# Performance work log

Measured on AMD Instinct MI355X. Metric: run time of the kernel, lower is better.

## Reference

```python
import jax, jax.numpy as jnp
import numpy as np

E = 2048        # embedding_dim
H = 16          # num_q_heads
G = 4           # group_size
HKV = H // G    # num_kv_heads = 4
D = E // H      # q_head_dim = 128
KVD = E // G    # kv_head_dim = 512
B, N = 2, 2048


def setup_inputs() -> dict:
    key = jax.random.key(0)
    ks = jax.random.split(key, 5)
    s = 0.02
    return {
        "x": jax.random.normal(ks[0], (B, N, E), jnp.float32),
        "Wq": jax.random.normal(ks[1], (E, E), jnp.float32) * s,
        "Wk": jax.random.normal(ks[2], (KVD, E), jnp.float32) * s,
        "Wv": jax.random.normal(ks[3], (KVD, E), jnp.float32) * s,
        "Wo": jax.random.normal(ks[4], (E, E), jnp.float32) * s,
    }


def reference(x, Wq, Wk, Wv, Wo):
    b, n, _ = x.shape
    # projections (nn.Linear: y = x @ W.T)
    q = x @ Wq.T                              # (b, n, E)
    k = x @ Wk.T                              # (b, n, KVD)
    v = x @ Wv.T                              # (b, n, KVD)
    # split heads: q -> b h n d with h=H, then (h g) -> g,h layout
    q = q.reshape(b, n, H, D).transpose(0, 2, 1, 3)          # b H n d
    q = q.reshape(b, HKV, G, n, D).transpose(0, 2, 1, 3, 4)  # b g h n d  (h=HKV)
    k = k.reshape(b, n, HKV, D).transpose(0, 2, 1, 3)        # b h s d
    v = v.reshape(b, n, HKV, D).transpose(0, 2, 1, 3)        # b h s d
    scale = 1.0 / jnp.sqrt(jnp.asarray(D, x.dtype))
    scores = jnp.einsum('bghnd,bhsd->bghns', q, k) * scale   # full score tensor
    scores = jax.nn.softmax(scores, axis=-1)
    # dropout p=0.0 -> identity
    o = jnp.einsum('bghns,bhsd->bghnd', scores, v)           # b g h n d
    # rearrange 'b g h n d -> b n (h g) d' then concat heads
    o = o.transpose(0, 3, 2, 1, 4).reshape(b, n, E)          # b n (h g) d -> b n E
    return o @ Wo.T
```

## Files before the change

### kernel.cpp

```cpp
#include <hip/hip_runtime.h>
#include <hip/hip_bf16.h>
#include <cstdint>
#include <cstddef>

using u16 = unsigned short;
typedef __bf16 bf16x8 __attribute__((ext_vector_type(8)));
typedef float f32x4 __attribute__((ext_vector_type(4)));
typedef float f32x16 __attribute__((ext_vector_type(16)));
typedef u16 u16x4 __attribute__((ext_vector_type(4)));
typedef u16 u16x8 __attribute__((ext_vector_type(8)));
typedef uint32_t u32x4 __attribute__((ext_vector_type(4)));

__device__ __forceinline__ u16 f2bf(float f) {
  uint32_t u = __builtin_bit_cast(uint32_t, f);
  u += 0x7FFFu + ((u >> 16) & 1u);
  return (u16)(u >> 16);
}

__device__ __forceinline__ void gld_lds16(const void* g, void* l) {
  __builtin_amdgcn_global_load_lds(
      (const __attribute__((address_space(1))) unsigned int*)g,
      (__attribute__((address_space(3))) unsigned int*)l, 16, 0, 0);
}

#define MFMA16(a, b, c) __builtin_amdgcn_mfma_f32_16x16x32_bf16((a), (b), (c), 0, 0, 0)
#define MFMA32(a, b, c) __builtin_amdgcn_mfma_f32_32x32x16_bf16((a), (b), (c), 0, 0, 0)

__device__ __forceinline__ uint32_t pkbf(float a, float b) {
  uint32_t d;
  asm("v_cvt_pk_bf16_f32 %0, %1, %2" : "=v"(d) : "v"(a), "v"(b));
  return d;
}
__device__ __forceinline__ void swap32(uint32_t& a, uint32_t& b) {
  asm volatile("v_permlane32_swap_b32 %0, %1" : "+v"(a), "+v"(b));
}

__global__ void cvt_kernel(const float* __restrict__ in, u16* __restrict__ out, int n4) {
  int i = blockIdx.x * blockDim.x + threadIdx.x;
  int stride = gridDim.x * blockDim.x;
  for (; i < n4; i += stride) {
    float4 v = reinterpret_cast<const float4*>(in)[i];
    u16x4 o;
    o[0] = f2bf(v.x); o[1] = f2bf(v.y); o[2] = f2bf(v.z); o[3] = f2bf(v.w);
    reinterpret_cast<u16x4*>(out)[i] = o;
  }
}

template <bool OUT_BF16>
__global__ __launch_bounds__(256) void gemm_bt(const u16* __restrict__ A,
                                               const u16* __restrict__ B,
                                               void* __restrict__ Cv,
                                               int M, int N, int K) {
  __shared__ __align__(16) u16 Ash[128 * 32];
  __shared__ __align__(16) u16 Bsh[128 * 32];
  const int tid = threadIdx.x;
  const int w = tid >> 6, lane = tid & 63, ql = lane & 15, g = lane >> 4;
  const int wr = w >> 1, wc = w & 1;
  const int m0 = blockIdx.y * 128, n0 = blockIdx.x * 128;
  const int srow = w * 16 + (lane >> 2);
  const int sk = (lane & 3) * 8;
  const u16* Abase = A + (size_t)(m0 + srow) * K + sk;
  const u16* Bbase = B + (size_t)(n0 + srow) * K + sk;

  f32x4 acc[4][4];
#pragma unroll
  for (int i = 0; i < 4; i++)
#pragma unroll
    for (int j = 0; j < 4; j++) acc[i][j] = f32x4{0.f, 0.f, 0.f, 0.f};

  for (int kt = 0; kt < K; kt += 32) {
    gld_lds16(Abase + kt,                  Ash + w * 512);
    gld_lds16(Abase + (size_t)64 * K + kt, Ash + 2048 + w * 512);
    gld_lds16(Bbase + kt,                  Bsh + w * 512);
    gld_lds16(Bbase + (size_t)64 * K + kt, Bsh + 2048 + w * 512);
    __syncthreads();
    bf16x8 af[4], bfr[4];
#pragma unroll
    for (int i = 0; i < 4; i++)
      af[i] = *reinterpret_cast<const bf16x8*>(&Ash[(wr * 64 + i * 16 + ql) * 32 + g * 8]);
#pragma unroll
    for (int j = 0; j < 4; j++)
      bfr[j] = *reinterpret_cast<const bf16x8*>(&Bsh[(wc * 64 + j * 16 + ql) * 32 + g * 8]);
#pragma unroll
    for (int i = 0; i < 4; i++)
#pragma unroll
      for (int j = 0; j < 4; j++)
        acc[i][j] = MFMA16(af[i], bfr[j], acc[i][j]);
    __syncthreads();
  }

#pragma unroll
  for (int i = 0; i < 4; i++)
#pragma unroll
    for (int j = 0; j < 4; j++)
#pragma unroll
      for (int r = 0; r < 4; r++) {
        const int row = m0 + wr * 64 + i * 16 + g * 4 + r;
        const int col = n0 + wc * 64 + j * 16 + ql;
        if constexpr (OUT_BF16)
          ((u16*)Cv)[(size_t)row * N + col] = f2bf(acc[i][j][r]);
        else
          ((float*)Cv)[(size_t)row * N + col] = acc[i][j][r];
      }
}

__global__ __launch_bounds__(256, 2) void attn_kernel(const u16* __restrict__ QKV,
                                                      u16* __restrict__ O) {
  __shared__ __align__(16) u16 Kb[2][64 * 128];
  __shared__ __align__(16) u16 Vb[2][2][128 * 32];
  const int tid = threadIdx.x, w = tid >> 6, lane = tid & 63;
  const int lq = lane & 31, hi = lane >> 5;
  const int qt = blockIdx.x;
  const int b = blockIdx.y >> 4, h = blockIdx.y & 15, hkv = h >> 2;
  const size_t rowb = (size_t)b * 2048;
  const int qbase = qt * 128 + w * 32;

  const u16* Kg = QKV + 2048 + hkv * 128;
  const u16* Vg = QKV + 2560 + hkv * 128;

  bf16x8 bq[8];
  {
    const u16* qp = QKV + (rowb + qbase + lq) * 3072 + h * 128 + hi * 8;
#pragma unroll
    for (int s5 = 0; s5 < 8; s5++)
      bq[s5] = *reinterpret_cast<const bf16x8*>(qp + s5 * 16);
  }

  const int dg = tid & 7, sl = tid >> 3;

  f32x16 oacc[4];
#pragma unroll
  for (int dt = 0; dt < 4; dt++)
#pragma unroll
    for (int i = 0; i < 16; i++) oacc[dt][i] = 0.f;
  float m = -INFINITY, l = 0.f;
  const float CEXP = 0.08838834764831845f * 1.4426950408889634f;

  auto stageK = [&](int pb2, int sbase) {
#pragma unroll
    for (int p = 0; p < 4; p++) {
      const int L = p * 2048 + tid * 8;
      const int s = L >> 7;
      const int gI = (L >> 3) & 15;
      gld_lds16(Kg + (rowb + sbase + s) * 3072 + ((gI ^ (s & 7)) << 3),
                &Kb[pb2][p * 2048 + w * 512]);
    }
  };
  auto writeV = [&](int pb2, const u16x8& a00, const u16x8& a01,
                    const u16x8& a10, const u16x8& a11) {
#pragma unroll
    for (int sh2 = 0; sh2 < 2; sh2++)
#pragma unroll
      for (int hf = 0; hf < 2; hf++) {
        const u16x8 v = sh2 ? (hf ? a11 : a10) : (hf ? a01 : a00);
#pragma unroll
        for (int j = 0; j < 8; j++) {
          const int d = dg * 16 + hf * 8 + j;
          const int key = ((d >> 1) ^ (d >> 4)) & 3;
          Vb[pb2][sh2][d * 32 + (sl ^ (key << 3))] = v[j];
        }
      }
  };

#define KFRAG(PB, SH, S5) \
  (*reinterpret_cast<const bf16x8*>(&Kb[PB][((SH)*32 + lq) * 128 + ((((S5)*2 + hi) ^ (lq & 7)) << 3)]))
#define VFRAG(PB, DT, SS) \
  (*reinterpret_cast<const bf16x8*>(&Vb[PB][(SS) >> 1][((DT)*32 + lq) * 32 + \
      ((((SS) & 1) * 16 + hi * 8) ^ (((((DT)*32 + lq) >> 1) ^ (((DT)*32 + lq) >> 4)) & 3) << 3)]))

  u16x8 v00, v01, v10, v11;
  {
    const u16* vp = Vg + (rowb + sl) * 3072 + dg * 16;
    v00 = *reinterpret_cast<const u16x8*>(vp);
    v01 = *reinterpret_cast<const u16x8*>(vp + 8);
    const u16* vp2 = vp + (size_t)32 * 3072;
    v10 = *reinterpret_cast<const u16x8*>(vp2);
    v11 = *reinterpret_cast<const u16x8*>(vp2 + 8);
  }
  stageK(0, 0);
  writeV(0, v00, v01, v10, v11);
  __syncthreads();

#pragma unroll 1
  for (int sb = 0; sb < 32; sb++) {
    const int pb = sb & 1;
    if (sb < 31) {
      const u16* vp = Vg + (rowb + (sb + 1) * 64 + sl) * 3072 + dg * 16;
      v00 = *reinterpret_cast<const u16x8*>(vp);
      v01 = *reinterpret_cast<const u16x8*>(vp + 8);
      const u16* vp2 = vp + (size_t)32 * 3072;
      v10 = *reinterpret_cast<const u16x8*>(vp2);
      v11 = *reinterpret_cast<const u16x8*>(vp2 + 8);
      stageK(pb ^ 1, (sb + 1) * 64);
    }

    f32x16 sc0, sc1;
#pragma unroll
    for (int i = 0; i < 16; i++) { sc0[i] = 0.f; sc1[i] = 0.f; }
    __builtin_amdgcn_s_setprio(1);
#pragma unroll
    for (int s5 = 0; s5 < 8; s5++) {
      sc0 = MFMA32(KFRAG(pb, 0, s5), bq[s5], sc0);
      sc1 = MFMA32(KFRAG(pb, 1, s5), bq[s5], sc1);
    }
    __builtin_amdgcn_s_setprio(0);

    float u[16];
#pragma unroll
    for (int i = 0; i < 16; i++) u[i] = fmaxf(sc0[i], sc1[i]);
#pragma unroll
    for (int i = 0; i < 8; i++) u[i] = fmaxf(u[i], u[i + 8]);
#pragma unroll
    for (int i = 0; i < 4; i++) u[i] = fmaxf(u[i], u[i + 4]);
    float mx = fmaxf(fmaxf(u[0], u[1]), fmaxf(u[2], u[3]));
    mx = fmaxf(mx, __shfl_xor(mx, 32));

    if (__any((mx - m) * CEXP > 8.0f)) {
      const float mn = fmaxf(m, mx);
      const float corr = exp2f((m - mn) * CEXP);
      l *= corr;
#pragma unroll
      for (int dt = 0; dt < 4; dt++)
#pragma unroll
        for (int i = 0; i < 16; i++) oacc[dt][i] *= corr;
      m = mn;
    }

    const float mC = m * CEXP;
    float e0[16], e1[16];
#pragma unroll
    for (int i = 0; i < 16; i++) {
      e0[i] = exp2f(fmaf(sc0[i], CEXP, -mC));
      e1[i] = exp2f(fmaf(sc1[i], CEXP, -mC));
    }
    float s[16];
#pragma unroll
    for (int i = 0; i < 16; i++) s[i] = e0[i] + e1[i];
#pragma unroll
    for (int i = 0; i < 8; i++) s[i] = s[i] + s[i + 8];
#pragma unroll
    for (int i = 0; i < 4; i++) s[i] = s[i] + s[i + 4];
    float ps = (s[0] + s[1]) + (s[2] + s[3]);
    ps += __shfl_xor(ps, 32);
    l += ps;

    bf16x8 pf0, pf1, pf2, pf3;
    {
      uint32_t a, bw;
      u32x4 f;
      a = pkbf(e0[0], e0[1]);  bw = pkbf(e0[4], e0[5]);  swap32(a, bw);
      f[0] = a; f[2] = bw;
      a = pkbf(e0[2], e0[3]);  bw = pkbf(e0[6], e0[7]);  swap32(a, bw);
      f[1] = a; f[3] = bw;
      pf0 = __builtin_bit_cast(bf16x8, f);
      a = pkbf(e0[8], e0[9]);  bw = pkbf(e0[12], e0[13]); swap32(a, bw);
      f[0] = a; f[2] = bw;
      a = pkbf(e0[10], e0[11]); bw = pkbf(e0[14], e0[15]); swap32(a, bw);
      f[1] = a; f[3] = bw;
      pf1 = __builtin_bit_cast(bf16x8, f);
      a = pkbf(e1[0], e1[1]);  bw = pkbf(e1[4], e1[5]);  swap32(a, bw);
      f[0] = a; f[2] = bw;
      a = pkbf(e1[2], e1[3]);  bw = pkbf(e1[6], e1[7]);  swap32(a, bw);
      f[1] = a; f[3] = bw;
      pf2 = __builtin_bit_cast(bf16x8, f);
      a = pkbf(e1[8], e1[9]);  bw = pkbf(e1[12], e1[13]); swap32(a, bw);
      f[0] = a; f[2] = bw;
      a = pkbf(e1[10], e1[11]); bw = pkbf(e1[14], e1[15]); swap32(a, bw);
      f[1] = a; f[3] = bw;
      pf3 = __builtin_bit_cast(bf16x8, f);
    }

    __builtin_amdgcn_s_setprio(1);
#pragma unroll
    for (int dt = 0; dt < 4; dt++) {
      oacc[dt] = MFMA32(VFRAG(pb, dt, 0), pf0, oacc[dt]);
      oacc[dt] = MFMA32(VFRAG(pb, dt, 1), pf1, oacc[dt]);
      oacc[dt] = MFMA32(VFRAG(pb, dt, 2), pf2, oacc[dt]);
      oacc[dt] = MFMA32(VFRAG(pb, dt, 3), pf3, oacc[dt]);
    }
    __builtin_amdgcn_s_setprio(0);

    if (sb < 31) writeV(pb ^ 1, v00, v01, v10, v11);
    __syncthreads();
  }

  const float rl = 1.0f / l;
  u16* ob = (w < 2) ? &Kb[w][0] : &Vb[w - 2][0][0];
#pragma unroll
  for (int dt = 0; dt < 4; dt++)
#pragma unroll
    for (int rq = 0; rq < 4; rq++) {
      u16x4 pv;
#pragma unroll
      for (int k = 0; k < 4; k++) pv[k] = f2bf(oacc[dt][rq * 4 + k] * rl);
      *reinterpret_cast<u16x4*>(&ob[lq * 136 + dt * 32 + rq * 8 + hi * 4]) = pv;
    }
  const int orow = lane >> 1, och = (lane & 1) * 64;
  u16* og = O + (rowb + qbase + orow) * 2048 + h * 128 + och;
#pragma unroll
  for (int t = 0; t < 8; t++) {
    u16x8 v = *reinterpret_cast<const u16x8*>(&ob[orow * 136 + och + t * 8]);
    *reinterpret_cast<u16x8*>(og + t * 8) = v;
  }
#undef KFRAG
#undef VFRAG
}

extern "C" void kernel_launch(void* const* d_in, const int* in_sizes, int n_in,
                              void* d_out, int out_size, void* d_ws, size_t ws_size,
                              hipStream_t stream) {
  (void)in_sizes; (void)n_in; (void)out_size;
  const float* x  = (const float*)d_in[0];
  const float* Wq = (const float*)d_in[1];
  const float* Wk = (const float*)d_in[2];
  const float* Wv = (const float*)d_in[3];
  const float* Wo = (const float*)d_in[4];

  if (ws_size < (size_t)(8388608 + 6291456 + 12582912) * 2) return;
  u16* xb  = (u16*)d_ws;
  u16* Wc  = xb + 8388608;
  u16* QKV = Wc + 6291456;
  u16* Ob  = xb;

  cvt_kernel<<<2048, 256, 0, stream>>>(x,  xb, 2097152);
  cvt_kernel<<<2048, 256, 0, stream>>>(Wq, Wc, 1048576);
  cvt_kernel<<<1024, 256, 0, stream>>>(Wk, Wc + 4194304, 262144);
  cvt_kernel<<<1024, 256, 0, stream>>>(Wv, Wc + 5242880, 262144);
  gemm_bt<true><<<dim3(24, 32), 256, 0, stream>>>(xb, Wc, (void*)QKV, 4096, 3072, 2048);
  cvt_kernel<<<2048, 256, 0, stream>>>(Wo, Wc, 1048576);
  attn_kernel<<<dim3(16, 32), 256, 0, stream>>>(QKV, Ob);
  gemm_bt<false><<<dim3(16, 32), 256, 0, stream>>>(Ob, Wc, d_out, 4096, 2048, 2048);
}
```

Before: 250.2 us.

## Triple-buffer GEMM LDS tiles with async prefetch two stages ahead

Turns the bf16 GEMM's single-buffered LDS tile loop into a three-stage ring. Global-to-LDS loads for tile t+2 are issued before computing tile t, and fine-grained vmcnt waits with one barrier per iteration replace the two __syncthreads. This is meant to hide global load latency behind MFMA work. It also raises wave priority around the MFMA block, and in exchange triples LDS use to 48KB per block, which may reduce occupancy.

After: 237.3 us. 5.1% less time.

```diff
diff --git a/kernel.cpp b/kernel.cpp
--- a/kernel.cpp
+++ b/kernel.cpp
@@ -51,8 +51,8 @@
                                                const u16* __restrict__ B,
                                                void* __restrict__ Cv,
                                                int M, int N, int K) {
-  __shared__ __align__(16) u16 Ash[128 * 32];
-  __shared__ __align__(16) u16 Bsh[128 * 32];
+  __shared__ __align__(16) u16 Ash[3][128 * 32];
+  __shared__ __align__(16) u16 Bsh[3][128 * 32];
   const int tid = threadIdx.x;
   const int w = tid >> 6, lane = tid & 63, ql = lane & 15, g = lane >> 4;
   const int wr = w >> 1, wc = w & 1;
@@ -68,25 +68,53 @@
 #pragma unroll
     for (int j = 0; j < 4; j++) acc[i][j] = f32x4{0.f, 0.f, 0.f, 0.f};
 
-  for (int kt = 0; kt < K; kt += 32) {
-    gld_lds16(Abase + kt,                  Ash + w * 512);
-    gld_lds16(Abase + (size_t)64 * K + kt, Ash + 2048 + w * 512);
-    gld_lds16(Bbase + kt,                  Bsh + w * 512);
-    gld_lds16(Bbase + (size_t)64 * K + kt, Bsh + 2048 + w * 512);
-    __syncthreads();
+  auto stage = [&](int bi, int tile) {
+    const int kt = tile * 32;
+    gld_lds16(Abase + kt,                  &Ash[bi][w * 512]);
+    gld_lds16(Abase + (size_t)64 * K + kt, &Ash[bi][2048 + w * 512]);
+    gld_lds16(Bbase + kt,                  &Bsh[bi][w * 512]);
+    gld_lds16(Bbase + (size_t)64 * K + kt, &Bsh[bi][2048 + w * 512]);
+  };
+
+  const int nt = K >> 5;
+  stage(0, 0);
+  stage(1, 1);
+  asm volatile("s_waitcnt vmcnt(4)" ::: "memory");
+  __builtin_amdgcn_sched_barrier(0);
+  __builtin_amdgcn_s_barrier();
+  __builtin_amdgcn_sched_barrier(0);
+
+  int cur = 0;
+  for (int t = 0; t < nt; ++t) {
+    if (t + 2 < nt) {
+      int stg = cur + 2; if (stg >= 3) stg -= 3;
+      stage(stg, t + 2);
+    }
     bf16x8 af[4], bfr[4];
 #pragma unroll
     for (int i = 0; i < 4; i++)
-      af[i] = *reinterpret_cast<const bf16x8*>(&Ash[(wr * 64 + i * 16 + ql) * 32 + g * 8]);
+      af[i] = *reinterpret_cast<const bf16x8*>(&Ash[cur][(wr * 64 + i * 16 + ql) * 32 + g * 8]);
 #pragma unroll
     for (int j = 0; j < 4; j++)
-      bfr[j] = *reinterpret_cast<const bf16x8*>(&Bsh[(wc * 64 + j * 16 + ql) * 32 + g * 8]);
+      bfr[j] = *reinterpret_cast<const bf16x8*>(&Bsh[cur][(wc * 64 + j * 16 + ql) * 32 + g * 8]);
+    __builtin_amdgcn_s_setprio(1);
 #pragma unroll
     for (int i = 0; i < 4; i++)
 #pragma unroll
       for (int j = 0; j < 4; j++)
         acc[i][j] = MFMA16(af[i], bfr[j], acc[i][j]);
-    __syncthreads();
+    __builtin_amdgcn_s_setprio(0);
+    if (t + 1 < nt) {
+      if (t + 2 < nt) {
+        asm volatile("s_waitcnt vmcnt(4)" ::: "memory");
+      } else {
+        asm volatile("s_waitcnt vmcnt(0)" ::: "memory");
+      }
+      __builtin_amdgcn_sched_barrier(0);
+      __builtin_amdgcn_s_barrier();
+      __builtin_amdgcn_sched_barrier(0);
+    }
+    cur = (cur == 2) ? 0 : cur + 1;
   }
 
 #pragma unroll
```
